# Kernel tuning notes

Measured on AMD Instinct MI355X. Metric: run time of the kernel, lower is better.

## Reference

```python
import jax, jax.numpy as jnp
import numpy as np

N = 50000      # nodes
E = 800000     # edges (before self-loops)
NG = 64        # graphs
H, C = 4, 32   # heads, out channels per head
D = 128        # feature dim == H*C
GS, K = 4, 3   # grid_size, spline_order
NB = GS + K    # number of B-spline bases = 7
NC = 10        # classes
L = 3          # gnn layers

# uniform KAN grid over [-1,1] extended by spline_order on each side
GRID = jnp.arange(-K, GS + K + 1, dtype=jnp.float32) * (2.0 / GS) - 1.0  # [GS+2K+1]


def b_splines(x, grid, k):
    # x: [N, in] -> bases: [N, in, GS+k] via Cox-de Boor recursion
    xe = x[..., None]
    bases = ((xe >= grid[:-1]) & (xe < grid[1:])).astype(x.dtype)
    for p in range(1, k + 1):
        left = (xe - grid[:-(p + 1)]) / (grid[p:-1] - grid[:-(p + 1)]) * bases[..., :-1]
        right = (grid[p + 1:] - xe) / (grid[p + 1:] - grid[1:-p]) * bases[..., 1:]
        bases = left + right
    return bases


def kan_linear(x, base_w, spline_w, scaler):
    # efficient-kan: silu(x)@base_w.T + b_splines(x) contracted with scaled spline weights
    base = jax.nn.silu(x) @ base_w.T
    bs = b_splines(x, GRID, K)                      # [N, in, NB]
    sw = spline_w * scaler[..., None]               # [out, in, NB]
    return base + jnp.einsum('nib,oib->no', bs, sw)


def gat_layer(x, src, dst, base_w, spline_w, scaler, att_src, att_dst, bias):
    n = x.shape[0]
    h = kan_linear(x, base_w, spline_w, scaler).reshape(n, H, C)
    a_src = jnp.sum(h * att_src, axis=-1)           # [N, H]
    a_dst = jnp.sum(h * att_dst, axis=-1)           # [N, H]
    e = jax.nn.leaky_relu(a_src[src] + a_dst[dst], 0.2)  # [Etot, H]
    # segment softmax over incoming edges of each destination node
    m = jax.ops.segment_max(e, dst, num_segments=n)
    ex = jnp.exp(e - m[dst])
    s = jax.ops.segment_sum(ex, dst, num_segments=n)
    alpha = ex / (s[dst] + 1e-16)                   # [Etot, H]
    msg = h[src] * alpha[..., None]                 # [Etot, H, C]
    out = jax.ops.segment_sum(msg, dst, num_segments=n)
    return out.reshape(n, H * C) + bias


def setup_inputs() -> dict:
    key = jax.random.key(0)
    ks = jax.random.split(key, 16)
    inp = {
        'x': jax.random.normal(ks[0], (N, D), dtype=jnp.float32),
        'edge_index': jax.random.randint(ks[1], (2, E), 0, N, dtype=jnp.int32),
        'batch': jnp.sort(jax.random.randint(ks[2], (N,), 0, NG, dtype=jnp.int32)),
        # stacked per-layer GAT+KAN params (all layers are [128 -> 128])
        'base_w': jax.random.normal(ks[3], (L, D, D), dtype=jnp.float32) * 0.05,
        'spline_w': jax.random.normal(ks[4], (L, D, D, NB), dtype=jnp.float32) * 0.05,
        'scaler': jax.random.normal(ks[5], (L, D, D), dtype=jnp.float32) * 0.3 + 1.0,
        'att_src': jax.random.normal(ks[6], (L, H, C), dtype=jnp.float32) * 0.1,
        'att_dst': jax.random.normal(ks[7], (L, H, C), dtype=jnp.float32) * 0.1,
        'bias': jnp.zeros((L, H * C), dtype=jnp.float32),
        # readout KANLinear [128 -> 10]
        'ro_base_w': jax.random.normal(ks[8], (NC, D), dtype=jnp.float32) * 0.05,
        'ro_spline_w': jax.random.normal(ks[9], (NC, D, NB), dtype=jnp.float32) * 0.05,
        'ro_scaler': jax.random.normal(ks[10], (NC, D), dtype=jnp.float32) * 0.3 + 1.0,
    }
    return inp


def reference(x, edge_index, batch, base_w, spline_w, scaler, att_src, att_dst, bias,
              ro_base_w, ro_spline_w, ro_scaler):
    # PyG GATConv default: add self-loops
    loops = jnp.arange(N, dtype=edge_index.dtype)
    src = jnp.concatenate([edge_index[0], loops])
    dst = jnp.concatenate([edge_index[1], loops])
    h = x
    for i in range(L):
        h = gat_layer(h, src, dst, base_w[i], spline_w[i], scaler[i],
                      att_src[i], att_dst[i], bias[i])
        h = jax.nn.silu(h)  # dropout is identity in eval mode
    pooled = jax.ops.segment_sum(h, batch, num_segments=NG)   # global_add_pool [NG, D]
    logits = kan_linear(pooled, ro_base_w, ro_spline_w, ro_scaler)
    return jax.nn.log_softmax(logits, axis=1)
```

## Files before the change

kernel.cpp:

```cpp
#include <hip/hip_runtime.h>
#include <math.h>

#define NN 50000
#define EE 800000
#define ETOT (EE + NN)
#define NGR 64
#define DD 128
#define NCL 10

#define NBUK 128
#define BNODES 391
#define P1CH 3321
#define P2CAP 8704

typedef __attribute__((ext_vector_type(16))) float float16_t;
typedef __attribute__((ext_vector_type(8)))  __bf16 bf16x8;

__device__ __forceinline__ float siluf(float x){ return x / (1.f + __expf(-x)); }

__device__ __forceinline__ unsigned f2bf(float f){
  union { float f; unsigned u; } v; v.f = f;
  unsigned r = v.u + 0x7fffu + ((v.u >> 16) & 1u);
  return (r >> 16) & 0xffffu;
}

__device__ __forceinline__ void kan_feats(float x, float* f8){
  f8[0] = siluf(x);
  float u = 2.f*x + 5.f;
  int cell = -1;
  float n0=0.f,n1=0.f,n2=0.f,n3=0.f;
  if (u >= 0.f && u < 10.f){
    cell = (int)u;
    float t = u - (float)cell;
    float t2 = t*t, t3 = t2*t;
    float omt = 1.f - t;
    const float s6 = 1.f/6.f;
    n0 = t3*s6;
    n1 = s6*(1.f + 3.f*t + 3.f*t2 - 3.f*t3);
    n2 = s6*(4.f - 6.f*t2 + 3.f*t3);
    n3 = omt*omt*omt*s6;
  }
#pragma unroll
  for (int j=0;j<7;++j){
    int k = cell - j;
    float v = (k==0)?n0:((k==1)?n1:((k==2)?n2:((k==3)?n3:0.f)));
    f8[1+j] = v;
  }
}

__device__ __forceinline__ int4 kan_feats_pack(float x){
  unsigned sbf = f2bf(siluf(x));
  float u = 2.f*x + 5.f;
  bool valid = (u >= 0.f) && (u < 10.f);
  float uc = valid ? u : 0.f;
  int cell = (int)uc;
  float t = uc - (float)cell;
  float t2 = t*t, t3 = t2*t, omt = 1.f - t;
  const float s6 = 1.f/6.f;
  float n0 = t3*s6;
  float n1 = s6*(1.f + 3.f*t + 3.f*t2 - 3.f*t3);
  float n2 = s6*(4.f - 6.f*t2 + 3.f*t3);
  float n3 = omt*omt*omt*s6;
  unsigned p0=f2bf(n0), p1=f2bf(n1), p2=f2bf(n2), p3=f2bf(n3);
  unsigned long long P = ((unsigned long long)(p1 | (p0<<16)) << 32)
                       |  (unsigned long long)(p3 | (p2<<16));
  int sh = cell*16 - 48;
  unsigned long long shl    = P << (sh & 63);
  unsigned long long shrhi  = P >> ((64 - sh) & 63);
  unsigned long long shllo2 = P << ((sh - 64) & 63);
  unsigned long long shrlo  = P >> ((-sh) & 63);
  unsigned long long F0, F1;
  if (sh < 0)       { F0 = shrlo; F1 = 0ull; }
  else if (sh < 64) { F0 = shl;   F1 = (sh==0)? 0ull : shrhi; }
  else              { F0 = 0ull;  F1 = shllo2; }
  if (!valid){ F0 = 0ull; F1 = 0ull; }
  unsigned w0 = ((unsigned)(F0 & 0xffffull) << 16) | sbf;
  unsigned w1 = (unsigned)((F0 >> 16) & 0xffffffffull);
  unsigned w2 = (unsigned)((F0 >> 48) & 0xffffull) | (((unsigned)(F1 & 0xffffull)) << 16);
  unsigned w3 = (unsigned)((F1 >> 16) & 0xffffffffull);
  return make_int4((int)w0,(int)w1,(int)w2,(int)w3);
}

__global__ void hist_kernel(const int* __restrict__ ei, int* __restrict__ deg){
  int e = blockIdx.x*256 + threadIdx.x;
  if (e >= ETOT) return;
  int dst = (e < EE) ? ei[EE + e] : (e - EE);
  atomicAdd(&deg[dst], 1);
}

__global__ void scan1_kernel(const int* __restrict__ deg, int* __restrict__ offs, int* __restrict__ part){
  __shared__ int sh[256];
  int tid = threadIdx.x;
  int i = blockIdx.x*256 + tid;
  int v = (i < NN) ? deg[i] : 0;
  sh[tid] = v; __syncthreads();
  for (int o=1;o<256;o<<=1){
    int t2 = (tid >= o) ? sh[tid - o] : 0;
    __syncthreads();
    sh[tid] += t2;
    __syncthreads();
  }
  int incl = sh[tid];
  if (i < NN) offs[i] = incl - v;
  if (tid == 255) part[blockIdx.x] = incl;
}

__global__ void scan2_kernel(int* __restrict__ part, int nb){
  __shared__ int sh[256];
  int tid = threadIdx.x;
  int v = (tid < nb) ? part[tid] : 0;
  sh[tid] = v; __syncthreads();
  for (int o=1;o<256;o<<=1){
    int t2 = (tid >= o) ? sh[tid - o] : 0;
    __syncthreads();
    sh[tid] += t2;
    __syncthreads();
  }
  if (tid < nb) part[tid] = sh[tid] - v;
}

__global__ void scan3_kernel(int* __restrict__ offs, const int* __restrict__ part, int* __restrict__ cursor){
  int i = blockIdx.x*256 + threadIdx.x;
  if (i >= NN) return;
  int o = offs[i] + part[blockIdx.x];
  offs[i] = o;
  cursor[i] = o;
}

__global__ void binit_kernel(const int* __restrict__ offs, int* __restrict__ bcur){
  int b = threadIdx.x;
  if (b < NBUK) bcur[b] = offs[b*BNODES];
}

__global__ __launch_bounds__(256) void binpass_kernel(const int* __restrict__ ei,
                                                      int* __restrict__ bcur,
                                                      unsigned* __restrict__ tmp){
  __shared__ int cnt[NBUK], lexcl[NBUK], gbase[NBUK], lcur[NBUK];
  __shared__ int sc[NBUK];
  __shared__ unsigned entries[P1CH + 7];
  const int t = threadIdx.x;
  const int e0 = blockIdx.x * P1CH;
  int e1 = e0 + P1CH; if (e1 > ETOT) e1 = ETOT;
  const int total = e1 - e0;

  if (t < NBUK){ cnt[t] = 0; lcur[t] = 0; }
  __syncthreads();

  unsigned myE[14]; int myB[14]; int myN = 0;
  for (int e = e0 + t; e < e1; e += 256){
    int src, dst;
    if (e < EE){ src = ei[e]; dst = ei[EE + e]; } else { src = e - EE; dst = src; }
    int b = dst / BNODES;
    int dl = dst - b*BNODES;
    myE[myN] = ((unsigned)b << 25) | ((unsigned)dl << 16) | (unsigned)src;
    myB[myN] = b;
    myN++;
    atomicAdd(&cnt[b], 1);
  }
  __syncthreads();

  if (t < NBUK) sc[t] = cnt[t];
  __syncthreads();
  for (int o=1;o<NBUK;o<<=1){
    int v = 0;
    if (t < NBUK && t >= o) v = sc[t - o];
    __syncthreads();
    if (t < NBUK) sc[t] += v;
    __syncthreads();
  }
  if (t < NBUK) lexcl[t] = sc[t] - cnt[t];
  __syncthreads();

  if (t < NBUK && cnt[t] > 0) gbase[t] = atomicAdd(&bcur[t], cnt[t]);
  __syncthreads();

  for (int k=0;k<myN;++k){
    int b = myB[k];
    int r = lexcl[b] + atomicAdd(&lcur[b], 1);
    entries[r] = myE[k];
  }
  __syncthreads();

  for (int s = t; s < total; s += 256){
    unsigned en = entries[s];
    int b = en >> 25;
    int pos = gbase[b] + (s - lexcl[b]);
    tmp[pos] = en;
  }
}

__global__ __launch_bounds__(256) void scatter_kernel(const unsigned* __restrict__ tmp,
                                                      const int* __restrict__ offs,
                                                      int* __restrict__ cursor,
                                                      int* __restrict__ csr){
  __shared__ unsigned ebuf[P2CAP];
  __shared__ unsigned sbuf[P2CAP];
  __shared__ int dcnt[BNODES+1], dscan[BNODES+1], dcur[BNODES+1];
  __shared__ int sA[512], sB[512];
  const int t = threadIdx.x;
  const int b = blockIdx.x;
  const int lo = b * BNODES;
  const int start = offs[lo];
  const int end = (b < NBUK-1) ? offs[lo + BNODES] : ETOT;
  const int cnt = end - start;

  if (cnt > P2CAP){
    for (int i = t; i < cnt; i += 256){
      unsigned en = tmp[start + i];
      int node = lo + (int)((en >> 16) & 0x1FF);
      int pos = atomicAdd(&cursor[node], 1);
      csr[pos] = (int)(en & 0xFFFF);
    }
    return;
  }

  for (int i = t; i < cnt; i += 256) ebuf[i] = tmp[start + i];
  for (int i = t; i < BNODES+1; i += 256){ dcnt[i] = 0; dcur[i] = 0; }
  __syncthreads();
  for (int i = t; i < cnt; i += 256){
    int dl = (ebuf[i] >> 16) & 0x1FF;
    atomicAdd(&dcnt[dl], 1);
  }
  __syncthreads();

  sA[t]       = (t       < BNODES+1) ? dcnt[t]       : 0;
  sA[t + 256] = (t + 256 < BNODES+1) ? dcnt[t + 256] : 0;
  __syncthreads();
  int* sp = sA; int* dp = sB;
  for (int o=1;o<512;o<<=1){
    dp[t]       = sp[t]       + ((t       >= o) ? sp[t - o]       : 0);
    dp[t + 256] = sp[t + 256] + ((t + 256 >= o) ? sp[t + 256 - o] : 0);
    __syncthreads();
    int* tpp = sp; sp = dp; dp = tpp;
  }
  if (t       < BNODES+1) dscan[t]       = sp[t]       - dcnt[t];
  if (t + 256 < BNODES+1) dscan[t + 256] = sp[t + 256] - dcnt[t + 256];
  __syncthreads();

  for (int i = t; i < cnt; i += 256){
    unsigned en = ebuf[i];
    int dl = (en >> 16) & 0x1FF;
    int r = dscan[dl] + atomicAdd(&dcur[dl], 1);
    sbuf[r] = en & 0xFFFFu;
  }
  __syncthreads();
  for (int i = t; i < cnt; i += 256) csr[start + i] = (int)sbuf[i];
}

__global__ void build_wfrag(const float* __restrict__ bw, const float* __restrict__ sw,
                            const float* __restrict__ sc, unsigned short* __restrict__ wfrag){
  int idx = blockIdx.x*256 + threadIdx.x;
  if (idx >= 3*128*1024) return;
  int k = idx & 1023;
  int o = (idx >> 10) & 127;
  int l = idx >> 17;
  int i = k >> 3, f = k & 7;
  int oi = (l*DD + o)*DD + i;
  float w = (f == 0) ? bw[oi] : sw[oi*7 + (f-1)] * sc[oi];
  int s = k >> 6;
  int sl = (k >> 4) & 3, half = (k >> 3) & 1, j = k & 7;
  int ntile = o >> 5, n = o & 31;
  int dst = l*131072 + s*8192 + (((ntile*4 + sl)*64) + half*32 + n)*8 + j;
  wfrag[dst] = (unsigned short)f2bf(w);
}

__global__ __launch_bounds__(256) void kan_gemm(const float* __restrict__ xin,
                                                const unsigned short* __restrict__ wfrag,
                                                const float* __restrict__ attS,
                                                const float* __restrict__ attD,
                                                unsigned int* __restrict__ hpack,
                                                float* __restrict__ asrc,
                                                float* __restrict__ adst, int layer)
{
  __shared__ __align__(16) float xs[64*132];
  __shared__ __align__(16) unsigned short Afrag[2][4096];
  const int t    = threadIdx.x;
  const int lane = t & 63;
  const int w    = t >> 6;
  const int half = lane >> 5;
  const int mn   = lane & 31;
  const int row0 = blockIdx.x * 64;
  const int r_my = t & 63;
  const int il0  = t >> 6;
  const unsigned short* wl = wfrag + layer*131072;

#pragma unroll
  for (int q=0;q<8;++q){
    int p = q*256 + t;
    int r = p >> 5, c4 = p & 31;
    int grow = row0 + r;
    float4 v = make_float4(0.f,0.f,0.f,0.f);
    if (grow < NN) v = *(const float4*)(xin + (size_t)grow*DD + c4*4);
    *(float4*)(&xs[r*132 + c4*4]) = v;
  }
  __syncthreads();

  float16_t acc[2];
#pragma unroll
  for (int i=0;i<16;++i){ acc[0][i]=0.f; acc[1][i]=0.f; }

  int4 Bc[4], Bn[4];
#pragma unroll
  for (int sl=0;sl<4;++sl)
    Bc[sl] = *(const int4*)(wl + ((w*4+sl)*64 + lane)*8);

  const int foa = (((r_my>>5)*8 + il0)*32 + (r_my&31))*8;
  const int fob = (((r_my>>5)*8 + il0+4)*32 + (r_my&31))*8;
  {
    int4 Pa = kan_feats_pack(xs[r_my*132 + il0]);
    int4 Pb = kan_feats_pack(xs[r_my*132 + il0 + 4]);
    *(int4*)(&Afrag[0][foa]) = Pa;
    *(int4*)(&Afrag[0][fob]) = Pb;
  }
  __syncthreads();

  for (int s=0; s<16; ++s){
    if (s < 15){
      const unsigned short* wsrc = wl + (s+1)*8192;
#pragma unroll
      for (int sl=0;sl<4;++sl)
        Bn[sl] = *(const int4*)(wsrc + ((w*4+sl)*64 + lane)*8);
      int4 Pa = kan_feats_pack(xs[r_my*132 + (s+1)*8 + il0]);
      int4 Pb = kan_feats_pack(xs[r_my*132 + (s+1)*8 + il0 + 4]);
      *(int4*)(&Afrag[(s+1)&1][foa]) = Pa;
      *(int4*)(&Afrag[(s+1)&1][fob]) = Pb;
    }
    const unsigned short* A = Afrag[s&1];
#pragma unroll
    for (int sl=0; sl<4; ++sl){
      int4 a0i = *(const int4*)(A + (((0*8 + sl*2 + half)*32) + mn)*8);
      int4 a1i = *(const int4*)(A + (((1*8 + sl*2 + half)*32) + mn)*8);
      bf16x8 b = __builtin_bit_cast(bf16x8, Bc[sl]);
      acc[0] = __builtin_amdgcn_mfma_f32_32x32x16_bf16(__builtin_bit_cast(bf16x8, a0i), b, acc[0], 0, 0, 0);
      acc[1] = __builtin_amdgcn_mfma_f32_32x32x16_bf16(__builtin_bit_cast(bf16x8, a1i), b, acc[1], 0, 0, 0);
    }
#pragma unroll
    for (int sl=0;sl<4;++sl) Bc[sl] = Bn[sl];
    __syncthreads();
  }

  unsigned short* hs = (unsigned short*)xs;
#pragma unroll
  for (int mt=0; mt<2; ++mt){
#pragma unroll
    for (int reg=0; reg<16; ++reg){
      int row = mt*32 + (reg&3) + 8*(reg>>2) + 4*half;
      int col = w*32 + mn;
      hs[row*136 + col] = (unsigned short)f2bf(acc[mt][reg]);
    }
  }
  __syncthreads();
#pragma unroll
  for (int q=0;q<4;++q){
    int p = q*256 + t;
    int row = p >> 4, u4 = p & 15;
    uint4 v = *(const uint4*)((const unsigned int*)(hs + row*136) + u4*4);
    int grow = row0 + row;
    if (grow < NN) *(uint4*)(hpack + (size_t)grow*64 + u4*4) = v;
  }
  {
    int r = t >> 2, h = t & 3;
    const unsigned* hrow = (const unsigned*)(hs + r*136) + h*16;
    const float* ws = attS + (layer*4 + h)*32;
    const float* wd = attD + (layer*4 + h)*32;
    float ss = 0.f, sd = 0.f;
#pragma unroll
    for (int j=0;j<16;++j){
      unsigned u = hrow[j];
      float flo = __uint_as_float(u << 16);
      float fhi = __uint_as_float(u & 0xffff0000u);
      ss += flo*ws[2*j] + fhi*ws[2*j+1];
      sd += flo*wd[2*j] + fhi*wd[2*j+1];
    }
    int grow = row0 + r;
    if (grow < NN){ asrc[grow*4 + h] = ss; adst[grow*4 + h] = sd; }
  }
}

__global__ __launch_bounds__(256) void attn_kernel(
    const unsigned int* __restrict__ hpack, const float* __restrict__ asrc, const float* __restrict__ adst,
    const int* __restrict__ offs, const int* __restrict__ deg, const int* __restrict__ csr,
    const float* __restrict__ bias, float* __restrict__ hout, int layer)
{
  const int wave = threadIdx.x >> 6;
  const int lane = threadIdx.x & 63;
  const int n = blockIdx.x*4 + wave;
  if (n >= NN) return;
  const int st = offs[n];
  const int d  = deg[n];
  const int eL = lane >> 2, h = lane & 3;
  const float adh = adst[n*4 + h];

  int   srcv[4];
  float ev[4];
  float mL = -3.4e38f;
#pragma unroll
  for (int c=0;c<4;++c){
    srcv[c] = 0; ev[c] = -3.4e38f;
    int e = c*16 + eL;
    if (e < d){
      int s2 = csr[st + e];
      srcv[c] = s2;
      float e0 = asrc[s2*4 + h] + adh;
      ev[c] = (e0 > 0.f) ? e0 : 0.2f*e0;
      mL = fmaxf(mL, ev[c]);
    }
  }
  for (int c=64; c<d; c+=16){
    int e = c + eL;
    if (e < d){
      int s2 = csr[st + e];
      float e0 = asrc[s2*4 + h] + adh;
      float evv = (e0 > 0.f) ? e0 : 0.2f*e0;
      mL = fmaxf(mL, evv);
    }
  }
#pragma unroll
  for (int o=4;o<64;o<<=1) mL = fmaxf(mL, __shfl_xor(mL, o));

  float av4[4];
  float sL = 0.f;
#pragma unroll
  for (int c=0;c<4;++c){ av4[c] = __expf(ev[c] - mL); sL += av4[c]; }
  for (int c=64; c<d; c+=16){
    int e = c + eL;
    if (e < d){
      int s2 = csr[st + e];
      float e0 = asrc[s2*4 + h] + adh;
      float evv = (e0 > 0.f) ? e0 : 0.2f*e0;
      sL += __expf(evv - mL);
    }
  }
#pragma unroll
  for (int o=4;o<64;o<<=1) sL += __shfl_xor(sL, o);
  const float inv = 1.f/(sL + 1e-16f);

  const int hq = lane >> 4;
  float accL = 0.f, accH = 0.f;
#pragma unroll
  for (int c=0;c<4;++c){
    if (c*16 < d){
      float ac = av4[c] * inv;
      int lim = d - c*16; if (lim > 16) lim = 16;
      unsigned uv[16]; float aj[16];
#pragma unroll
      for (int j=0;j<16;++j){
        int sj = __shfl(srcv[c], j*4);
        aj[j]  = __shfl(ac,      j*4 + hq);
        if (j < lim) uv[j] = hpack[(size_t)sj*64 + lane];
        else         uv[j] = 0u;
      }
#pragma unroll
      for (int j=0;j<16;++j){
        accL = fmaf(aj[j], __uint_as_float(uv[j] << 16),         accL);
        accH = fmaf(aj[j], __uint_as_float(uv[j] & 0xffff0000u), accH);
      }
    }
  }
  for (int c=64; c<d; c+=16){
    int e = c + eL;
    int s2 = 0; float al = 0.f;
    if (e < d){
      s2 = csr[st + e];
      float e0 = asrc[s2*4 + h] + adh;
      float evv = (e0 > 0.f) ? e0 : 0.2f*e0;
      al = __expf(evv - mL) * inv;
    }
    int lim = d - c; if (lim > 16) lim = 16;
    for (int j=0;j<lim;++j){
      int sj = __shfl(s2, j*4);
      float aH = __shfl(al, j*4 + hq);
      unsigned u = hpack[(size_t)sj*64 + lane];
      accL = fmaf(aH, __uint_as_float(u << 16),         accL);
      accH = fmaf(aH, __uint_as_float(u & 0xffff0000u), accH);
    }
  }
  float2 bv = *(const float2*)(bias + layer*DD + 2*lane);
  float o0 = siluf(accL + bv.x);
  float o1 = siluf(accH + bv.y);
  *(float2*)(hout + (size_t)n*DD + 2*lane) = make_float2(o0, o1);
}

__global__ __launch_bounds__(128) void pool_kernel(const float* __restrict__ h,
    const int* __restrict__ batch, float* __restrict__ pooled)
{
  int c = threadIdx.x;
  int n0 = blockIdx.x*128;
  float sum = 0.f; int cur = -1;
  for (int r=0;r<128;++r){
    int n = n0 + r;
    if (n >= NN) break;
    int g = batch[n];
    if (g != cur){
      if (cur >= 0) atomicAdd(&pooled[cur*DD + c], sum);
      cur = g; sum = 0.f;
    }
    sum += h[n*DD + c];
  }
  if (cur >= 0) atomicAdd(&pooled[cur*DD + c], sum);
}

__global__ __launch_bounds__(64) void readout_kernel(const float* __restrict__ pooled,
    const float* __restrict__ bw, const float* __restrict__ sw, const float* __restrict__ sc,
    float* __restrict__ out)
{
  int g = blockIdx.x, lane = threadIdx.x;
  float xa = pooled[g*DD + lane];
  float xb = pooled[g*DD + lane + 64];
  float fa[8], fb[8];
  kan_feats(xa, fa);
  kan_feats(xb, fb);
  float logits[NCL];
#pragma unroll
  for (int c=0;c<NCL;++c){
    int ia = c*DD + lane, ib = ia + 64;
    float sca = sc[ia], scb = sc[ib];
    float p = fa[0]*bw[ia] + fb[0]*bw[ib];
#pragma unroll
    for (int f=1;f<8;++f)
      p += fa[f]*sw[ia*7 + f-1]*sca + fb[f]*sw[ib*7 + f-1]*scb;
#pragma unroll
    for (int o=1;o<64;o<<=1) p += __shfl_xor(p, o);
    logits[c] = p;
  }
  float mx = logits[0];
#pragma unroll
  for (int c=1;c<NCL;++c) mx = fmaxf(mx, logits[c]);
  float lse = 0.f;
#pragma unroll
  for (int c=0;c<NCL;++c) lse += __expf(logits[c]-mx);
  lse = mx + logf(lse);
  if (lane < NCL){
    float v = 0.f;
#pragma unroll
    for (int c=0;c<NCL;++c) if (lane == c) v = logits[c] - lse;
    out[g*NCL + lane] = v;
  }
}

extern "C" void kernel_launch(void* const* d_in, const int* in_sizes, int n_in,
                              void* d_out, int out_size, void* d_ws, size_t ws_size,
                              hipStream_t stream)
{
  const float* x        = (const float*)d_in[0];
  const int*   ei       = (const int*)  d_in[1];
  const int*   batch    = (const int*)  d_in[2];
  const float* base_w   = (const float*)d_in[3];
  const float* spline_w = (const float*)d_in[4];
  const float* scaler   = (const float*)d_in[5];
  const float* att_src  = (const float*)d_in[6];
  const float* att_dst  = (const float*)d_in[7];
  const float* bias     = (const float*)d_in[8];
  const float* ro_bw    = (const float*)d_in[9];
  const float* ro_sw    = (const float*)d_in[10];
  const float* ro_sc    = (const float*)d_in[11];
  float* out = (float*)d_out;

  char* p = (char*)d_ws;
  auto alloc = [&](size_t bytes)->char* {
    char* r = p;
    p += (bytes + 255) & ~(size_t)255;
    return r;
  };
  unsigned int* hpack = (unsigned int*)alloc((size_t)50048*64*4);
  float* hbuf   = (float*)alloc((size_t)NN*DD*4);
  unsigned short* wfrag = (unsigned short*)alloc((size_t)3*131072*2);
  float* asrc   = (float*)alloc((size_t)NN*4*4);
  float* adst   = (float*)alloc((size_t)NN*4*4);
  float* pooled = (float*)alloc((size_t)NGR*DD*4);
  int*   deg    = (int*)alloc((size_t)NN*4);
  int*   offs   = (int*)alloc((size_t)NN*4);
  int*   cursor = (int*)alloc((size_t)NN*4);
  int*   csr    = (int*)alloc((size_t)ETOT*4);
  unsigned* tmp = (unsigned*)alloc((size_t)ETOT*4);
  int*   bcur   = (int*)alloc((size_t)NBUK*4);
  int*   part   = (int*)alloc((size_t)256*4);

  const int nbs = (NN + 255)/256;
  hipMemsetAsync(deg, 0, (size_t)NN*sizeof(int), stream);
  hist_kernel   <<<(ETOT+255)/256, 256, 0, stream>>>(ei, deg);
  scan1_kernel  <<<nbs, 256, 0, stream>>>(deg, offs, part);
  scan2_kernel  <<<1,   256, 0, stream>>>(part, nbs);
  scan3_kernel  <<<nbs, 256, 0, stream>>>(offs, part, cursor);
  binit_kernel  <<<1,   128, 0, stream>>>(offs, bcur);
  binpass_kernel<<<256, 256, 0, stream>>>(ei, bcur, tmp);
  scatter_kernel<<<NBUK,256, 0, stream>>>(tmp, offs, cursor, csr);
  build_wfrag   <<<(3*128*1024)/256, 256, 0, stream>>>(base_w, spline_w, scaler, wfrag);

  const float* cur = x;
  for (int l=0; l<3; ++l){
    kan_gemm   <<<(NN+63)/64, 256, 0, stream>>>(cur, wfrag, att_src, att_dst,
                                                hpack, asrc, adst, l);
    attn_kernel<<<(NN+3)/4,   256, 0, stream>>>(hpack, asrc, adst, offs, deg, csr,
                                                bias, hbuf, l);
    cur = hbuf;
  }
  hipMemsetAsync(pooled, 0, (size_t)NGR*DD*sizeof(float), stream);
  pool_kernel   <<<(NN+127)/128, 128, 0, stream>>>(hbuf, batch, pooled);
  readout_kernel<<<NGR, 64, 0, stream>>>(pooled, ro_bw, ro_sw, ro_sc, out);
}
```

Before: 459.7 us.

## Stream KAN GEMM inputs directly from global and drop x staging LDS

The kan_gemm kernel no longer stages the 64x128 float input tile in shared memory. Each thread now loads two adjacent feature values per K-step straight from global memory into registers, packs the spline features and writes them to the Afrag double buffer. The output bf16 tile reuses the Afrag buffer without padding and uses rotated column indexing to avoid bank conflicts. This cuts LDS use by about 33KB per block to allow higher occupancy and removes one barrier, at the cost of small strided global loads inside the main loop.

```diff
diff --git a/kernel.cpp b/kernel.cpp
--- a/kernel.cpp
+++ b/kernel.cpp
@@ -272,7 +272,6 @@
                                                 float* __restrict__ asrc,
                                                 float* __restrict__ adst, int layer)
 {
-  __shared__ __align__(16) float xs[64*132];
   __shared__ __align__(16) unsigned short Afrag[2][4096];
   const int t    = threadIdx.x;
   const int lane = t & 63;
@@ -280,20 +279,14 @@
   const int half = lane >> 5;
   const int mn   = lane & 31;
   const int row0 = blockIdx.x * 64;
-  const int r_my = t & 63;
-  const int il0  = t >> 6;
   const unsigned short* wl = wfrag + layer*131072;
 
-#pragma unroll
-  for (int q=0;q<8;++q){
-    int p = q*256 + t;
-    int r = p >> 5, c4 = p & 31;
-    int grow = row0 + r;
-    float4 v = make_float4(0.f,0.f,0.f,0.f);
-    if (grow < NN) v = *(const float4*)(xin + (size_t)grow*DD + c4*4);
-    *(float4*)(&xs[r*132 + c4*4]) = v;
-  }
-  __syncthreads();
+  const int row_l = t >> 2;
+  const int il_l  = (t & 3) * 2;
+  const int grow_l = row0 + row_l;
+  const float* xr = xin + (size_t)((grow_l < NN) ? grow_l : 0)*DD + il_l;
+  const int foa = (((row_l>>5)*8 + il_l  )*32 + (row_l&31))*8;
+  const int fob = foa + 256;
 
   float16_t acc[2];
 #pragma unroll
@@ -304,13 +297,10 @@
   for (int sl=0;sl<4;++sl)
     Bc[sl] = *(const int4*)(wl + ((w*4+sl)*64 + lane)*8);
 
-  const int foa = (((r_my>>5)*8 + il0)*32 + (r_my&31))*8;
-  const int fob = (((r_my>>5)*8 + il0+4)*32 + (r_my&31))*8;
   {
-    int4 Pa = kan_feats_pack(xs[r_my*132 + il0]);
-    int4 Pb = kan_feats_pack(xs[r_my*132 + il0 + 4]);
-    *(int4*)(&Afrag[0][foa]) = Pa;
-    *(int4*)(&Afrag[0][fob]) = Pb;
+    float2 xv = *(const float2*)(xr);
+    *(int4*)(&Afrag[0][foa]) = kan_feats_pack(xv.x);
+    *(int4*)(&Afrag[0][fob]) = kan_feats_pack(xv.y);
   }
   __syncthreads();
 
@@ -320,8 +310,9 @@
 #pragma unroll
       for (int sl=0;sl<4;++sl)
         Bn[sl] = *(const int4*)(wsrc + ((w*4+sl)*64 + lane)*8);
-      int4 Pa = kan_feats_pack(xs[r_my*132 + (s+1)*8 + il0]);
-      int4 Pb = kan_feats_pack(xs[r_my*132 + (s+1)*8 + il0 + 4]);
+      float2 xn = *(const float2*)(xr + (s+1)*8);
+      int4 Pa = kan_feats_pack(xn.x);
+      int4 Pb = kan_feats_pack(xn.y);
       *(int4*)(&Afrag[(s+1)&1][foa]) = Pa;
       *(int4*)(&Afrag[(s+1)&1][fob]) = Pb;
     }
@@ -339,38 +330,40 @@
     __syncthreads();
   }
 
-  unsigned short* hs = (unsigned short*)xs;
+  unsigned short* hs = (unsigned short*)Afrag;
 #pragma unroll
   for (int mt=0; mt<2; ++mt){
 #pragma unroll
     for (int reg=0; reg<16; ++reg){
       int row = mt*32 + (reg&3) + 8*(reg>>2) + 4*half;
       int col = w*32 + mn;
-      hs[row*136 + col] = (unsigned short)f2bf(acc[mt][reg]);
+      hs[row*128 + col] = (unsigned short)f2bf(acc[mt][reg]);
     }
   }
   __syncthreads();
 #pragma unroll
   for (int q=0;q<4;++q){
     int p = q*256 + t;
-    int row = p >> 4, u4 = p & 15;
-    uint4 v = *(const uint4*)((const unsigned int*)(hs + row*136) + u4*4);
+    int row = p >> 4;
+    int u4 = ((p & 15) + row) & 15;
+    uint4 v = *(const uint4*)((const unsigned int*)hs + row*64 + u4*4);
     int grow = row0 + row;
     if (grow < NN) *(uint4*)(hpack + (size_t)grow*64 + u4*4) = v;
   }
   {
     int r = t >> 2, h = t & 3;
-    const unsigned* hrow = (const unsigned*)(hs + r*136) + h*16;
+    const unsigned* hrow = (const unsigned*)hs + r*64 + h*16;
     const float* ws = attS + (layer*4 + h)*32;
     const float* wd = attD + (layer*4 + h)*32;
     float ss = 0.f, sd = 0.f;
 #pragma unroll
     for (int j=0;j<16;++j){
-      unsigned u = hrow[j];
+      int jj = (j + r) & 15;
+      unsigned u = hrow[jj];
       float flo = __uint_as_float(u << 16);
       float fhi = __uint_as_float(u & 0xffff0000u);
-      ss += flo*ws[2*j] + fhi*ws[2*j+1];
-      sd += flo*wd[2*j] + fhi*wd[2*j+1];
+      ss += flo*ws[2*jj] + fhi*ws[2*jj+1];
+      sd += flo*wd[2*jj] + fhi*wd[2*jj+1];
     }
     int grow = row0 + r;
     if (grow < NN){ asrc[grow*4 + h] = ss; adst[grow*4 + h] = sd; }
```

Result: slower. 485.2 us (+5.6%).
